# Kernel tuning notes

Hardware: AMD Instinct MI355X
Metric: run time of the kernel (lower is better)

## Reference

```python
import jax, jax.numpy as jnp
import numpy as np

# Grouped TF->gene sparse decoder dims
T = 512       # number of TFs (tf_size)
K = 4         # nodes_per_tf (width_multiplier); decoder_features = T*K = 2048
G = 20000     # number of genes (gene_size)
EPG = 3       # regulating TFs per gene (TF-gene edges per gene)
B = 512       # batch of cells


def setup_inputs() -> dict:
    key = jax.random.key(0)
    k0, k1, k2, k3, k4, k5, k6 = jax.random.split(key, 7)
    features = jax.random.normal(k0, (B, T), dtype=jnp.float32)
    # Layer 1: each TF fans out to its own K hidden nodes (one weight per edge)
    w1 = jax.random.normal(k1, (T, K), dtype=jnp.float32) * 0.5
    b1 = jax.random.normal(k2, (T, K), dtype=jnp.float32) * 0.1
    # Layer 2: block-dense KxK mixing within each TF group
    w2 = jax.random.normal(k3, (T, K, K), dtype=jnp.float32) * (1.0 / np.sqrt(K))
    b2 = jax.random.normal(k4, (T, K), dtype=jnp.float32) * 0.1
    # Output layer: gene g sums over its EPG TF edges x K hidden nodes
    w3 = jax.random.normal(k5, (G, EPG, K), dtype=jnp.float32) * (1.0 / np.sqrt(EPG * K))
    b3 = jax.random.normal(k6, (G,), dtype=jnp.float32) * 0.1
    # Fixed irregular TF-gene connectivity (constant structure, like data_obj)
    edge_tf = jnp.asarray(
        np.random.default_rng(0).integers(0, T, size=(G, EPG)), dtype=jnp.int32
    )
    return {"features": features, "w1": w1, "b1": b1, "w2": w2, "b2": b2,
            "w3": w3, "b3": b3, "edge_tf": edge_tf}


def reference(features, w1, b1, w2, b2, w3, b3, edge_tf):
    # SparseLinear decoder_1: TF t -> its K hidden nodes, then LeakyReLU(0.01)
    h1 = jax.nn.leaky_relu(features[:, :, None] * w1 + b1)            # [B,T,K]
    # SparseLinear decoder_2: block-dense within each TF group + LeakyReLU
    h2 = jax.nn.leaky_relu(jnp.einsum('btj,tjk->btk', h1, w2) + b2)   # [B,T,K]
    # SparseLinear output: gather each gene's regulating TF groups, contract
    gathered = h2[:, edge_tf, :]                                      # [B,G,EPG,K]
    out = jnp.einsum('bgek,gek->bg', gathered, w3) + b3               # [B,G]
    return out
```

## Files before the change

kernel.cpp:

```cpp
#include <hip/hip_runtime.h>

namespace {

constexpr int T = 512;
constexpr int K = 4;
constexpr int G = 20000;
constexpr int EPG = 3;
constexpr int B = 512;
constexpr int GB = 256;
constexpr int NXB = (G + GB - 1) / GB;
constexpr int GPAD = NXB * GB;
constexpr int BT = 4;
constexpr int NYB = 16;
constexpr int NTILE = B / (BT * NYB);
constexpr float SLOPE = 0.01f;
constexpr size_t H2T_OFF = 2u << 20;

__device__ __forceinline__ float lrelu(float x) { return x > 0.0f ? x : SLOPE * x; }

__global__ __launch_bounds__(256) void h2t_kernel(
    const float* __restrict__ features, const float* __restrict__ w1,
    const float* __restrict__ b1, const float* __restrict__ w2,
    const float* __restrict__ b2, float* __restrict__ h2t) {
  const int t = blockIdx.x;
  const int b = blockIdx.y * 256 + threadIdx.x;
  const float f = features[(size_t)b * T + t];
  const float4 W1 = reinterpret_cast<const float4*>(w1)[t];
  const float4 B1 = reinterpret_cast<const float4*>(b1)[t];
  const float4 B2 = reinterpret_cast<const float4*>(b2)[t];
  const float h0 = lrelu(f * W1.x + B1.x);
  const float h1 = lrelu(f * W1.y + B1.y);
  const float h2 = lrelu(f * W1.z + B1.z);
  const float h3 = lrelu(f * W1.w + B1.w);
  const float4* W2 = reinterpret_cast<const float4*>(w2 + (size_t)t * (K * K));
  const float4 r0 = W2[0];
  const float4 r1 = W2[1];
  const float4 r2 = W2[2];
  const float4 r3 = W2[3];
  float4 o;
  o.x = lrelu(B2.x + h0 * r0.x + h1 * r1.x + h2 * r2.x + h3 * r3.x);
  o.y = lrelu(B2.y + h0 * r0.y + h1 * r1.y + h2 * r2.y + h3 * r3.y);
  o.z = lrelu(B2.z + h0 * r0.z + h1 * r1.z + h2 * r2.z + h3 * r3.z);
  o.w = lrelu(B2.w + h0 * r0.w + h1 * r1.w + h2 * r2.w + h3 * r3.w);
  reinterpret_cast<float4*>(h2t)[(size_t)t * B + b] = o;
}

__global__ __launch_bounds__(256) void prep_kernel(
    const float* __restrict__ w3, const float* __restrict__ b3,
    const int* __restrict__ edge, float4* __restrict__ rec) {
  const int g = blockIdx.x * 256 + threadIdx.x;
  float4 a = make_float4(0.f, 0.f, 0.f, 0.f), b = a, c = a, d = a;
  if (g < G) {
    const float4* wp = reinterpret_cast<const float4*>(w3 + (size_t)g * (EPG * K));
    a = wp[0];
    b = wp[1];
    c = wp[2];
    d.x = b3[g];
    d.y = __int_as_float(edge[g * EPG + 0] * (BT * K * 4));
    d.z = __int_as_float(edge[g * EPG + 1] * (BT * K * 4));
    d.w = __int_as_float(edge[g * EPG + 2] * (BT * K * 4));
  } else {
    d.y = d.z = d.w = __int_as_float(0);
  }
  float4* o = rec + (size_t)g * 4;
  o[0] = a; o[1] = b; o[2] = c; o[3] = d;
}

__global__ __launch_bounds__(256, 4) void out_kernel_v4(
    const float* __restrict__ h2t, const float4* __restrict__ rec,
    float* __restrict__ out) {
  __shared__ float lds[BT * T * K];
  const int tid = threadIdx.x;
  const int gsub = tid >> 2;
  const int bidx = tid & 3;
  const int wid = tid >> 6;
  const int g0 = blockIdx.x * GB;
  const int b0 = blockIdx.y * (BT * NTILE);

  float4 rw0[4], rw1[4], rw2[4], rm[4];
#pragma unroll
  for (int s = 0; s < 4; ++s) {
    const float4* r = rec + (size_t)(g0 + s * 64 + gsub) * 4;
    rw0[s] = r[0]; rw1[s] = r[1]; rw2[s] = r[2]; rm[s] = r[3];
  }
  int off0[4], off1[4], off2[4];
#pragma unroll
  for (int s = 0; s < 4; ++s) {
    off0[s] = __float_as_int(rm[s].y) + bidx * 16;
    off1[s] = __float_as_int(rm[s].z) + bidx * 16;
    off2[s] = __float_as_int(rm[s].w) + bidx * 16;
  }

  const char* ldsc = reinterpret_cast<const char*>(lds);

  for (int ib = 0; ib < NTILE; ++ib) {
    const int bb = b0 + ib * BT;
#pragma unroll
    for (int j = 0; j < 8; ++j) {
      const int idx = j * 256 + tid;
      const int t = idx >> 2;
      const int b = idx & 3;
      const float* src = h2t + ((size_t)t * B + bb + b) * 4;
      char* dst = reinterpret_cast<char*>(lds) + (j * 256 + wid * 64) * 16;
      __builtin_amdgcn_global_load_lds(
          (const __attribute__((address_space(1))) void*)src,
          (__attribute__((address_space(3))) void*)dst, 16, 0, 0);
    }
    asm volatile("s_waitcnt vmcnt(0)" ::: "memory");
    __syncthreads();

#pragma unroll
    for (int s = 0; s < 4; ++s) {
      const float4 v0 = *reinterpret_cast<const float4*>(ldsc + off0[s]);
      const float4 v1 = *reinterpret_cast<const float4*>(ldsc + off1[s]);
      const float4 v2 = *reinterpret_cast<const float4*>(ldsc + off2[s]);
      float a = rm[s].x;
      a += v0.x * rw0[s].x + v0.y * rw0[s].y + v0.z * rw0[s].z + v0.w * rw0[s].w;
      a += v1.x * rw1[s].x + v1.y * rw1[s].y + v1.z * rw1[s].z + v1.w * rw1[s].w;
      a += v2.x * rw2[s].x + v2.y * rw2[s].y + v2.z * rw2[s].z + v2.w * rw2[s].w;
      const int g = g0 + s * 64 + gsub;
      if (g < G) out[(size_t)(bb + bidx) * G + g] = a;
    }
    __syncthreads();
  }
}

}

extern "C" void kernel_launch(void* const* d_in, const int* in_sizes, int n_in,
                              void* d_out, int out_size, void* d_ws, size_t ws_size,
                              hipStream_t stream) {
  const float* features = (const float*)d_in[0];
  const float* w1 = (const float*)d_in[1];
  const float* b1 = (const float*)d_in[2];
  const float* w2 = (const float*)d_in[3];
  const float* b2 = (const float*)d_in[4];
  const float* w3 = (const float*)d_in[5];
  const float* b3 = (const float*)d_in[6];
  const int* edge = (const int*)d_in[7];
  float* out = (float*)d_out;

  float4* rec = (float4*)d_ws;
  float* h2t = (float*)((char*)d_ws + H2T_OFF);

  dim3 g1(T, B / 256);
  h2t_kernel<<<g1, 256, 0, stream>>>(features, w1, b1, w2, b2, h2t);

  prep_kernel<<<GPAD / 256, 256, 0, stream>>>(w3, b3, edge, rec);

  dim3 g2(NXB, NYB);
  out_kernel_v4<<<g2, 256, 0, stream>>>(h2t, rec, out);
}
```

Before: 114.9 us.

## Restructure output kernel: one batch slab per block, loop over gene chunks

The output kernel now gives each block a 4-row batch slab, loaded once into padded LDS (row stride 20 floats to reduce bank conflicts). Each thread handles one gene for all 4 batch rows, iterating over gene chunks while prefetching the next chunk's weight record into registers. Before, each block held gene records in registers and reloaded the h2 slab through async global-to-LDS loads once per batch tile. The change aims to cut the repeated LDS refills and barriers and gain ILP, at the cost of more rec reads from global memory and plain staged loads instead of direct-to-LDS.

```diff
diff --git a/kernel.cpp b/kernel.cpp
--- a/kernel.cpp
+++ b/kernel.cpp
@@ -7,16 +7,20 @@
 constexpr int G = 20000;
 constexpr int EPG = 3;
 constexpr int B = 512;
-constexpr int GB = 256;
-constexpr int NXB = (G + GB - 1) / GB;
-constexpr int GPAD = NXB * GB;
 constexpr int BT = 4;
-constexpr int NYB = 16;
-constexpr int NTILE = B / (BT * NYB);
+constexpr int NSLAB = B / BT;
+constexpr int NG = 8;
+constexpr int GPB = 2560;
+constexpr int GPAD = NG * GPB;
+constexpr int NCHUNK = GPB / 256;
+constexpr int ROWSTRIDE = 20;
 constexpr float SLOPE = 0.01f;
 constexpr size_t H2T_OFF = 2u << 20;
 
 __device__ __forceinline__ float lrelu(float x) { return x > 0.0f ? x : SLOPE * x; }
+__device__ __forceinline__ float dot4(float4 a, float4 b) {
+  return a.x * b.x + a.y * b.y + a.z * b.z + a.w * b.w;
+}
 
 __global__ __launch_bounds__(256) void h2t_kernel(
     const float* __restrict__ features, const float* __restrict__ w1,
@@ -56,9 +60,9 @@
     b = wp[1];
     c = wp[2];
     d.x = b3[g];
-    d.y = __int_as_float(edge[g * EPG + 0] * (BT * K * 4));
-    d.z = __int_as_float(edge[g * EPG + 1] * (BT * K * 4));
-    d.w = __int_as_float(edge[g * EPG + 2] * (BT * K * 4));
+    d.y = __int_as_float(edge[g * EPG + 0] * (ROWSTRIDE * 4));
+    d.z = __int_as_float(edge[g * EPG + 1] * (ROWSTRIDE * 4));
+    d.w = __int_as_float(edge[g * EPG + 2] * (ROWSTRIDE * 4));
   } else {
     d.y = d.z = d.w = __int_as_float(0);
   }
@@ -66,62 +70,69 @@
   o[0] = a; o[1] = b; o[2] = c; o[3] = d;
 }
 
-__global__ __launch_bounds__(256, 4) void out_kernel_v4(
+__global__ __launch_bounds__(256, 4) void out_kernel_v5(
     const float* __restrict__ h2t, const float4* __restrict__ rec,
     float* __restrict__ out) {
-  __shared__ float lds[BT * T * K];
+  __shared__ float lds[T * ROWSTRIDE];
   const int tid = threadIdx.x;
-  const int gsub = tid >> 2;
-  const int bidx = tid & 3;
-  const int wid = tid >> 6;
-  const int g0 = blockIdx.x * GB;
-  const int b0 = blockIdx.y * (BT * NTILE);
+  const int b0 = blockIdx.x * BT;
+  const int gbase = blockIdx.y * GPB;
 
-  float4 rw0[4], rw1[4], rw2[4], rm[4];
 #pragma unroll
-  for (int s = 0; s < 4; ++s) {
-    const float4* r = rec + (size_t)(g0 + s * 64 + gsub) * 4;
-    rw0[s] = r[0]; rw1[s] = r[1]; rw2[s] = r[2]; rm[s] = r[3];
+  for (int it = 0; it < (T * BT) / 256; ++it) {
+    const int flat = it * 256 + tid;
+    const int t = flat >> 2;
+    const int b = flat & 3;
+    const float4 v = reinterpret_cast<const float4*>(h2t)[(size_t)t * B + b0 + b];
+    *reinterpret_cast<float4*>(&lds[t * ROWSTRIDE + b * 4]) = v;
   }
-  int off0[4], off1[4], off2[4];
-#pragma unroll
-  for (int s = 0; s < 4; ++s) {
-    off0[s] = __float_as_int(rm[s].y) + bidx * 16;
-    off1[s] = __float_as_int(rm[s].z) + bidx * 16;
-    off2[s] = __float_as_int(rm[s].w) + bidx * 16;
-  }
+  __syncthreads();
 
   const char* ldsc = reinterpret_cast<const char*>(lds);
 
-  for (int ib = 0; ib < NTILE; ++ib) {
-    const int bb = b0 + ib * BT;
-#pragma unroll
-    for (int j = 0; j < 8; ++j) {
-      const int idx = j * 256 + tid;
-      const int t = idx >> 2;
-      const int b = idx & 3;
-      const float* src = h2t + ((size_t)t * B + bb + b) * 4;
-      char* dst = reinterpret_cast<char*>(lds) + (j * 256 + wid * 64) * 16;
-      __builtin_amdgcn_global_load_lds(
-          (const __attribute__((address_space(1))) void*)src,
-          (__attribute__((address_space(3))) void*)dst, 16, 0, 0);
+  float4 p0, p1, p2, p3;
+  {
+    const float4* r = rec + (size_t)(gbase + tid) * 4;
+    p0 = r[0]; p1 = r[1]; p2 = r[2]; p3 = r[3];
+  }
+  for (int s = 0; s < NCHUNK; ++s) {
+    const float4 c0 = p0, c1 = p1, c2 = p2, c3 = p3;
+    const int g = gbase + s * 256 + tid;
+    if (s + 1 < NCHUNK) {
+      const float4* r = rec + (size_t)(gbase + (s + 1) * 256 + tid) * 4;
+      p0 = r[0]; p1 = r[1]; p2 = r[2]; p3 = r[3];
     }
-    asm volatile("s_waitcnt vmcnt(0)" ::: "memory");
-    __syncthreads();
-
-#pragma unroll
-    for (int s = 0; s < 4; ++s) {
-      const float4 v0 = *reinterpret_cast<const float4*>(ldsc + off0[s]);
-      const float4 v1 = *reinterpret_cast<const float4*>(ldsc + off1[s]);
-      const float4 v2 = *reinterpret_cast<const float4*>(ldsc + off2[s]);
-      float a = rm[s].x;
-      a += v0.x * rw0[s].x + v0.y * rw0[s].y + v0.z * rw0[s].z + v0.w * rw0[s].w;
-      a += v1.x * rw1[s].x + v1.y * rw1[s].y + v1.z * rw1[s].z + v1.w * rw1[s].w;
-      a += v2.x * rw2[s].x + v2.y * rw2[s].y + v2.z * rw2[s].z + v2.w * rw2[s].w;
-      const int g = g0 + s * 64 + gsub;
-      if (g < G) out[(size_t)(bb + bidx) * G + g] = a;
+    const int o0 = __float_as_int(c3.y);
+    const int o1 = __float_as_int(c3.z);
+    const int o2 = __float_as_int(c3.w);
+    float a0 = c3.x, a1 = c3.x, a2 = c3.x, a3 = c3.x;
+    {
+      const float4 v0 = *reinterpret_cast<const float4*>(ldsc + o0);
+      const float4 v1 = *reinterpret_cast<const float4*>(ldsc + o0 + 16);
+      const float4 v2 = *reinterpret_cast<const float4*>(ldsc + o0 + 32);
+      const float4 v3 = *reinterpret_cast<const float4*>(ldsc + o0 + 48);
+      a0 += dot4(v0, c0); a1 += dot4(v1, c0); a2 += dot4(v2, c0); a3 += dot4(v3, c0);
     }
-    __syncthreads();
+    {
+      const float4 v0 = *reinterpret_cast<const float4*>(ldsc + o1);
+      const float4 v1 = *reinterpret_cast<const float4*>(ldsc + o1 + 16);
+      const float4 v2 = *reinterpret_cast<const float4*>(ldsc + o1 + 32);
+      const float4 v3 = *reinterpret_cast<const float4*>(ldsc + o1 + 48);
+      a0 += dot4(v0, c1); a1 += dot4(v1, c1); a2 += dot4(v2, c1); a3 += dot4(v3, c1);
+    }
+    {
+      const float4 v0 = *reinterpret_cast<const float4*>(ldsc + o2);
+      const float4 v1 = *reinterpret_cast<const float4*>(ldsc + o2 + 16);
+      const float4 v2 = *reinterpret_cast<const float4*>(ldsc + o2 + 32);
+      const float4 v3 = *reinterpret_cast<const float4*>(ldsc + o2 + 48);
+      a0 += dot4(v0, c2); a1 += dot4(v1, c2); a2 += dot4(v2, c2); a3 += dot4(v3, c2);
+    }
+    if (g < G) {
+      out[(size_t)(b0 + 0) * G + g] = a0;
+      out[(size_t)(b0 + 1) * G + g] = a1;
+      out[(size_t)(b0 + 2) * G + g] = a2;
+      out[(size_t)(b0 + 3) * G + g] = a3;
+    }
   }
 }
 
@@ -148,6 +159,6 @@
 
   prep_kernel<<<GPAD / 256, 256, 0, stream>>>(w3, b3, edge, rec);
 
-  dim3 g2(NXB, NYB);
-  out_kernel_v4<<<g2, 256, 0, stream>>>(h2t, rec, out);
+  dim3 g2(NSLAB, NG);
+  out_kernel_v5<<<g2, 256, 0, stream>>>(h2t, rec, out);
 }
```

After: 100.2 us. 12.8% less time.
